# Kernel tuning notes

Hardware: AMD Instinct MI355X
Metric: run time of the kernel (lower is better)

The kernel has to match this reference:

```python
import jax, jax.numpy as jnp
import numpy as np

DIM = 64; N_LAYER = 2; B = 2048; M = 64
N_ENT = 100000; N_REL = 200
TEMP = 0.2; KGE_W = 1e-6
MIN_N = 1e-15; BND = 1e-5


def _norm(x):
    return jnp.sqrt(jnp.clip((x * x).sum(-1, keepdims=True), MIN_N))


def _l2(x):
    # F.normalize(p=2): x / max(||x||, 1e-12)
    return x / jnp.maximum(jnp.sqrt((x * x).sum(-1, keepdims=True)), 1e-12)


def _artanh(x):
    return jnp.arctanh(jnp.clip(x, -1.0 + BND, 1.0 - BND))


def expmap0(u):
    n = _norm(u)
    return jnp.tanh(n) * u / n


def logmap0(x):
    n = _norm(x)
    return _artanh(n) * x / n


def mobius_add(x, y):
    x2 = (x * x).sum(-1, keepdims=True)
    y2 = (y * y).sum(-1, keepdims=True)
    xy = (x * y).sum(-1, keepdims=True)
    num = (1 + 2 * xy + y2) * x + (1 - x2) * y
    den = 1 + 2 * xy + x2 * y2
    return num / jnp.clip(den, MIN_N)


def expmap(u, p):
    lam = 2.0 / jnp.clip(1.0 - (p * p).sum(-1, keepdims=True), MIN_N)
    n = _norm(u)
    return mobius_add(p, jnp.tanh(lam * n / 2.0) * u / n)


def logmap(x, p):
    m = mobius_add(-p, x)
    n = _norm(m)
    lam = 2.0 / jnp.clip(1.0 - (p * p).sum(-1, keepdims=True), MIN_N)
    return (2.0 / lam) * _artanh(n) * m / n


def _ed_agg(h, path, t, att_w1, att_w2):
    # attention: Linear(2d,d,no bias) -> LeakyReLU(0)==ReLU -> Linear(d,1,no bias) -> Sigmoid
    x = jnp.concatenate([h, path], -1)                       # [B,M,2d]
    a = jax.nn.sigmoid(jax.nn.relu(x @ att_w1) @ att_w2)[..., 0]  # [B,M]
    w = jax.nn.softmax(a, axis=-1)
    return (w[..., None] * t).sum(1)                          # [B,d]


def _hyper_agg(h, path, t, curvature, a2_w1, a2_b1, a2_w2, a2_b2):
    h, path, t = _l2(h), _l2(path), _l2(t)
    hh = expmap0(h) * jnp.abs(curvature)
    ht = expmap(t, hh)
    hr = expmap(path, hh)
    tang = logmap0(jnp.concatenate([hh, hr], -1))            # [B,M,2d]
    a = jnp.tanh(jax.nn.relu(tang @ a2_w1 + a2_b1) @ a2_w2 + a2_b2)[..., 0]
    w = jax.nn.softmax(a, axis=-1)                            # [B,M]
    agg = w[..., None] * ht
    mean_pt = (w[..., None] * hh).sum(1, keepdims=True)       # [B,1,d]
    e = logmap(agg, mean_pt)
    return (w[..., None] * e).sum(1)                          # [B,d]


def _build(E, R, h_idx, r_idx, t_idx, init_emb, agg):
    embs = [init_emb]
    for i in range(N_LAYER):
        h = E[h_idx[0]]
        path = R[r_idx[0]]
        for k in range(1, i + 1):  # faithful to source: inner loop reuses index i
            h = h + E[h_idx[i]]
            path = path * R[r_idx[i]]
        embs.append(agg(h, path, E[t_idx[i]]))
    return jnp.stack(embs)  # [L+1, B, d]


def _mlcl(a_stack, b_stack):
    # vectorized over layer index i of MLCL_Loss(a[i], b[i], a_list, b_list)
    na, nb = _l2(a_stack), _l2(b_stack)                       # [L+1,B,d]
    d = na.shape[-1]
    pos = (na * nb).sum(-1)                                   # [L+1,B]
    ttl1 = jnp.einsum('lbd,md->lbm', na, nb.reshape(-1, d))
    ttl2 = jnp.einsum('lbd,md->lbm', nb, na.reshape(-1, d))
    ep = jnp.exp(pos / TEMP)
    l1 = -jnp.log(ep / jnp.exp(ttl1 / TEMP).sum(-1)).sum()
    l2 = -jnp.log(ep / jnp.exp(ttl2 / TEMP).sum(-1)).sum()
    return KGE_W * (l1 + l2)


def _cat_rev(stack):
    # e = stack[0]; for i in 1..L: e = cat(stack[i], e) -> [L, L-1, ..., 0]
    return jnp.concatenate([stack[i] for i in range(stack.shape[0] - 1, -1, -1)], -1)


def setup_inputs() -> dict:
    key = jax.random.key(0)
    ks = jax.random.split(key, 24)
    def ent_idx(k):
        return jax.random.randint(k, (N_LAYER, B, M), 0, N_ENT, dtype=jnp.int32)
    def rel_idx(k):
        return jax.random.randint(k, (N_LAYER, B, M), 0, N_REL, dtype=jnp.int32)
    inp = {
        'items': jax.random.randint(ks[0], (B,), 0, N_ENT, dtype=jnp.int32),
        'ucf_h': ent_idx(ks[1]), 'ucf_r': rel_idx(ks[2]), 'ucf_t': ent_idx(ks[3]),
        'ikg_h': ent_idx(ks[4]), 'ikg_r': rel_idx(ks[5]), 'ikg_t': ent_idx(ks[6]),
        'ukg_h': ent_idx(ks[7]), 'ukg_r': rel_idx(ks[8]), 'ukg_t': ent_idx(ks[9]),
        'icf_h': ent_idx(ks[10]), 'icf_r': rel_idx(ks[11]), 'icf_t': ent_idx(ks[12]),
        'ent_emb': jax.random.normal(ks[13], (N_ENT, DIM), jnp.float32) * 0.02,
        'rel_emb': jax.random.normal(ks[14], (N_REL, DIM), jnp.float32) * 0.02,
        'att_w1': jax.random.normal(ks[15], (2 * DIM, DIM), jnp.float32) * 0.05,
        'att_w2': jax.random.normal(ks[16], (DIM, 1), jnp.float32) * 0.05,
        'att2_w1': jax.random.normal(ks[17], (2 * DIM, DIM), jnp.float32) * 0.05,
        'att2_b1': jnp.zeros((DIM,), jnp.float32),
        'att2_w2': jax.random.normal(ks[18], (DIM, 1), jnp.float32) * 0.05,
        'att2_b2': jnp.zeros((1,), jnp.float32),
        'curvature': jnp.asarray(1.0, jnp.float32),
    }
    return inp


def reference(items, ucf_h, ucf_r, ucf_t, ikg_h, ikg_r, ikg_t,
              ukg_h, ukg_r, ukg_t, icf_h, icf_r, icf_t,
              ent_emb, rel_emb, att_w1, att_w2,
              att2_w1, att2_b1, att2_w2, att2_b2, curvature):
    ed = lambda h, p, t: _ed_agg(h, p, t, att_w1, att_w2)
    hy = lambda h, p, t: _hyper_agg(h, p, t, curvature, att2_w1, att2_b1, att2_w2, att2_b2)
    ucf = _build(ent_emb, rel_emb, ucf_h, ucf_r, ucf_t, ent_emb[ucf_h[0]].mean(1), ed)
    ikg = _build(ent_emb, rel_emb, ikg_h, ikg_r, ikg_t, ent_emb[items], ed)
    ukg = _build(ent_emb, rel_emb, ukg_h, ukg_r, ukg_t, ent_emb[ukg_h[0]].mean(1), hy)
    icf = _build(ent_emb, rel_emb, icf_h, icf_r, icf_t, ent_emb[icf_h[0]].mean(1), hy)
    kge_loss = _mlcl(ucf, ukg) + _mlcl(ikg, icf)
    e_u = jnp.concatenate([_cat_rev(ucf), _cat_rev(ukg)], -1)
    e_i = jnp.concatenate([_cat_rev(icf), _cat_rev(ikg)], -1)
    scores = jax.nn.sigmoid((e_i * e_u).sum(-1))
    return scores, kge_loss
```

## Files before the change

kernel.cpp:

```cpp
#include <hip/hip_runtime.h>
#include <hip/hip_bf16.h>
#include <cstdint>
#include <cstddef>

constexpr int NB = 2048;
constexpr int NM = 64;
constexpr int ND = 64;
constexpr int NBM = NB * NM;
constexpr int NROWS = 3 * NB;
constexpr int STACK = 3 * NB * ND;
constexpr int NZ = 8;

typedef __attribute__((ext_vector_type(8))) short short8;
typedef __attribute__((ext_vector_type(4))) float float4v;

__device__ __forceinline__ float wsum(float v) {
#pragma unroll
  for (int o = 32; o > 0; o >>= 1) v += __shfl_xor(v, o, 64);
  return v;
}

__device__ __forceinline__ float wmax(float v) {
#pragma unroll
  for (int o = 32; o > 0; o >>= 1) v = fmaxf(v, __shfl_xor(v, o, 64));
  return v;
}

__device__ __forceinline__ float rcpf(float x) { return __builtin_amdgcn_rcpf(x); }
__device__ __forceinline__ float sqf(float x) { return __builtin_amdgcn_sqrtf(x); }

__device__ __forceinline__ float fast_tanh(float x) {
  float t = __expf(2.f * x);
  return (t - 1.f) * rcpf(t + 1.f);
}

__device__ __forceinline__ float artanh_clip(float x) {
  x = fminf(fmaxf(x, -1.f + 1e-5f), 1.f - 1e-5f);
  return 0.5f * __logf((1.f + x) * rcpf(1.f - x));
}

__device__ __forceinline__ ushort f2bf(float f) {
  uint u = __float_as_uint(f);
  return (ushort)((u + 0x7FFFu + ((u >> 16) & 1u)) >> 16);
}
__device__ __forceinline__ float bf2f(ushort u) {
  return __uint_as_float((uint)u << 16);
}

__device__ __forceinline__ float readlane_f(float v, int l) {
  return __int_as_float(__builtin_amdgcn_readlane(__float_as_int(v), l));
}

__global__ __launch_bounds__(256) void pack_w1_kernel(
    const float* __restrict__ w1, ushort* __restrict__ out) {
  int e = blockIdx.x * 256 + threadIdx.x;
  if (e >= 8192) return;
  int j = e & 7, ln = (e >> 3) & 63, nt = (e >> 9) & 3, kt = e >> 11;
  int n = nt * 16 + (ln & 15), k = kt * 32 + ((ln >> 4) << 3) + j;
  out[e] = f2bf(w1[k * 64 + n]);
}

__global__ __launch_bounds__(64) void init_item_kernel(
    const float* __restrict__ E, const int* __restrict__ idx, float* __restrict__ out) {
  int b = blockIdx.x, lane = threadIdx.x;
  out[(size_t)b * ND + lane] = E[(size_t)idx[b] * ND + lane];
}

__global__ __launch_bounds__(256) void ed_agg2_kernel(
    const float* __restrict__ E, const float* __restrict__ R,
    const int* __restrict__ h_idx, const int* __restrict__ r_idx,
    const int* __restrict__ t_idx,
    const ushort* __restrict__ w1p, const float* __restrict__ w2,
    float* __restrict__ stack_base, int do_init) {
  __shared__ __align__(16) __hip_bfloat16 xt[64][136];
  __shared__ float a_s[64];
  __shared__ float w_s[64];
  __shared__ float part[4][64];

  const int b = blockIdx.x;
  const int tid = threadIdx.x;
  const int wave = tid >> 6, lane = tid & 63;
  const int m0 = __builtin_amdgcn_readfirstlane(wave) * 16;
  const int colq = lane & 15, quad = lane >> 4;
  const size_t L = (size_t)NB * ND;

  float hd[16], pd[16];

  for (int layer = 0; layer < 2; ++layer) {
    if (layer == 0) {
      float macc = 0.f;
#pragma unroll
      for (int mi = 0; mi < 16; ++mi) {
        const int m = m0 + mi;
        hd[mi] = E[(size_t)h_idx[b * NM + m] * ND + lane];
        pd[mi] = R[(size_t)r_idx[b * NM + m] * ND + lane];
        macc += hd[mi];
        xt[m][lane] = __float2bfloat16(hd[mi]);
        xt[m][64 + lane] = __float2bfloat16(pd[mi]);
      }
      part[wave][lane] = macc;
      __syncthreads();
      if (do_init && wave == 0)
        stack_base[(size_t)b * ND + lane] =
            (part[0][lane] + part[1][lane] + part[2][lane] + part[3][lane]) * (1.f / 64.f);
    } else {
#pragma unroll
      for (int mi = 0; mi < 16; ++mi) {
        const int m = m0 + mi;
        hd[mi] += E[(size_t)h_idx[NBM + b * NM + m] * ND + lane];
        pd[mi] *= R[(size_t)r_idx[NBM + b * NM + m] * ND + lane];
        xt[m][lane] = __float2bfloat16(hd[mi]);
        xt[m][64 + lane] = __float2bfloat16(pd[mi]);
      }
      __syncthreads();
    }

    {
      short8 afr[4];
#pragma unroll
      for (int kt = 0; kt < 4; ++kt)
        afr[kt] = *(const short8*)&xt[m0 + colq][kt * 32 + quad * 8];
      float w2v[4];
#pragma unroll
      for (int nt = 0; nt < 4; ++nt) w2v[nt] = w2[nt * 16 + colq];
      float cc[4][4];
#pragma unroll
      for (int nt = 0; nt < 4; ++nt) {
        float4v c = {0.f, 0.f, 0.f, 0.f};
#pragma unroll
        for (int kt = 0; kt < 4; ++kt) {
          short8 bfr = *(const short8*)&w1p[(((kt << 2) | nt) * 64 + lane) * 8];
          c = __builtin_amdgcn_mfma_f32_16x16x32_bf16(afr[kt], bfr, c, 0, 0, 0);
        }
#pragma unroll
        for (int i = 0; i < 4; ++i) cc[nt][i] = c[i];
      }
      float sred[4];
#pragma unroll
      for (int i = 0; i < 4; ++i)
        sred[i] = fmaxf(cc[0][i], 0.f) * w2v[0] + fmaxf(cc[1][i], 0.f) * w2v[1] +
                  fmaxf(cc[2][i], 0.f) * w2v[2] + fmaxf(cc[3][i], 0.f) * w2v[3];
#pragma unroll
      for (int o = 8; o > 0; o >>= 1) {
#pragma unroll
        for (int i = 0; i < 4; ++i) sred[i] += __shfl_xor(sred[i], o, 64);
      }
      if (colq == 0) {
#pragma unroll
        for (int i = 0; i < 4; ++i)
          a_s[m0 + quad * 4 + i] = 1.f / (1.f + __expf(-sred[i]));
      }
    }
    __syncthreads();
    if (wave == 0) {
      float v = a_s[lane];
      float mx = wmax(v);
      float e = __expf(v - mx);
      float ssum = wsum(e);
      w_s[lane] = e / ssum;
    }
    __syncthreads();

    float o = 0.f;
#pragma unroll
    for (int mi = 0; mi < 16; ++mi) {
      const int m = m0 + mi;
      o = fmaf(w_s[m], E[(size_t)t_idx[(size_t)layer * NBM + b * NM + m] * ND + lane], o);
    }
    part[wave][lane] = o;
    __syncthreads();
    if (wave == 0)
      stack_base[(layer + 1) * L + (size_t)b * ND + lane] =
          part[0][lane] + part[1][lane] + part[2][lane] + part[3][lane];
  }
}

constexpr int OFF_T2 = 0;
constexpr int OFF_P2 = 64 * 72;
constexpr int OFF_H2 = 2 * 64 * 72;
constexpr int XS = 152;
constexpr int OFF_HTS = 64 * XS;
constexpr int REGA_SZ = OFF_HTS + 64 * 72;

__global__ __launch_bounds__(256) void hyper_agg2_kernel(
    const float* __restrict__ E, const float* __restrict__ R,
    const int* __restrict__ h_idx, const int* __restrict__ r_idx,
    const int* __restrict__ t_idx,
    const ushort* __restrict__ w1p, const float* __restrict__ b1,
    const float* __restrict__ w2, const float* __restrict__ b2,
    const float* __restrict__ curv, float* __restrict__ stack_base) {
  __shared__ __align__(16) ushort regA[REGA_SZ];
  __shared__ float dots_s[5][64];
  __shared__ float a_s[64];
  __shared__ float w_s[64];
  __shared__ float meanpt_s[64];
  __shared__ float part[4][64];
  __shared__ float scal;

  const int b = blockIdx.x;
  const int tid = threadIdx.x;
  const int wave = tid >> 6, lane = tid & 63;
  const int m0 = __builtin_amdgcn_readfirstlane(wave) * 16;
  const int colq = lane & 15, quad = lane >> 4;
  const float cabs = fabsf(*curv);
  const size_t L = (size_t)NB * ND;

  float hv[16], pv[16];

  for (int layer = 0; layer < 2; ++layer) {
    if (layer == 0) {
      float macc = 0.f;
#pragma unroll
      for (int mi = 0; mi < 16; ++mi) {
        const int m = m0 + mi;
        hv[mi] = E[(size_t)h_idx[b * NM + m] * ND + lane];
        pv[mi] = R[(size_t)r_idx[b * NM + m] * ND + lane];
        float td = E[(size_t)t_idx[b * NM + m] * ND + lane];
        macc += hv[mi];
        regA[OFF_H2 + m * 72 + lane] = f2bf(hv[mi]);
        regA[OFF_P2 + m * 72 + lane] = f2bf(pv[mi]);
        regA[OFF_T2 + m * 72 + lane] = f2bf(td);
      }
      part[wave][lane] = macc;
      __syncthreads();
      if (wave == 0)
        stack_base[(size_t)b * ND + lane] =
            (part[0][lane] + part[1][lane] + part[2][lane] + part[3][lane]) * (1.f / 64.f);
    } else {
#pragma unroll
      for (int mi = 0; mi < 16; ++mi) {
        const int m = m0 + mi;
        hv[mi] += E[(size_t)h_idx[NBM + b * NM + m] * ND + lane];
        pv[mi] *= R[(size_t)r_idx[NBM + b * NM + m] * ND + lane];
        float td = E[(size_t)t_idx[(size_t)NBM + b * NM + m] * ND + lane];
        regA[OFF_H2 + m * 72 + lane] = f2bf(hv[mi]);
        regA[OFF_P2 + m * 72 + lane] = f2bf(pv[mi]);
        regA[OFF_T2 + m * 72 + lane] = f2bf(td);
      }
      __syncthreads();
    }

    {
      const int fr = m0 + colq;
      const ushort* pH = &regA[OFF_H2 + fr * 72 + quad * 8];
      const ushort* pP = &regA[OFF_P2 + fr * 72 + quad * 8];
      const ushort* pT = &regA[OFF_T2 + fr * 72 + quad * 8];
      short8 h0 = *(const short8*)pH, h1 = *(const short8*)(pH + 32);
      short8 p0 = *(const short8*)pP, p1 = *(const short8*)(pP + 32);
      short8 t0 = *(const short8*)pT, t1 = *(const short8*)(pT + 32);
      const bool dsel = (quad == (colq >> 2));
      const int dr = colq & 3;
#define DIAG_DOT(q, A0, A1, B0, B1)                                         \
      {                                                                      \
        float4v c = {0.f, 0.f, 0.f, 0.f};                                    \
        c = __builtin_amdgcn_mfma_f32_16x16x32_bf16(A0, B0, c, 0, 0, 0);     \
        c = __builtin_amdgcn_mfma_f32_16x16x32_bf16(A1, B1, c, 0, 0, 0);     \
        float dv = (dr & 2) ? ((dr & 1) ? c[3] : c[2])                       \
                            : ((dr & 1) ? c[1] : c[0]);                      \
        if (dsel) dots_s[q][m0 + colq] = dv;                                 \
      }
      DIAG_DOT(0, h0, h1, h0, h1)
      DIAG_DOT(1, p0, p1, p0, p1)
      DIAG_DOT(2, t0, t1, t0, t1)
      DIAG_DOT(3, h0, h1, t0, t1)
      DIAG_DOT(4, h0, h1, p0, p1)
#undef DIAG_DOT
    }
    __syncthreads();

    float g_ch, g_e1, g_e2, g_gh, g_q1, g_q2, g_hts2;
    {
      const int mm = lane;
      float sh = dots_s[0][mm], sp = dots_s[1][mm], st = dots_s[2][mm];
      float sht = dots_s[3][mm], shp = dots_s[4][mm];
      float rih = rcpf(fmaxf(sqf(sh), 1e-12f));
      float rip = rcpf(fmaxf(sqf(sp), 1e-12f));
      float rit = rcpf(fmaxf(sqf(st), 1e-12f));
      float nh = sqf(fmaxf(sh * rih * rih, 1e-15f));
      float ch = fast_tanh(nh) * rcpf(nh) * rih * cabs;
      float p2 = ch * ch * sh;
      float lam = 2.f * rcpf(fmaxf(1.f - p2, 1e-15f));
      float ntn = sqf(fmaxf(st * rit * rit, 1e-15f));
      float ct = fast_tanh(0.5f * lam * ntn) * rcpf(ntn) * rit;
      float y2 = ct * ct * st, xy = ch * ct * sht;
      float At = 1.f + 2.f * xy + y2, Bt = 1.f - p2;
      float rdt = rcpf(fmaxf(1.f + 2.f * xy + p2 * y2, 1e-15f));
      g_e1 = At * ch * rdt;
      g_e2 = Bt * ct * rdt;
      g_hts2 = g_e1 * g_e1 * sh + 2.f * g_e1 * g_e2 * sht + g_e2 * g_e2 * st;
      float npn = sqf(fmaxf(sp * rip * rip, 1e-15f));
      float cp = fast_tanh(0.5f * lam * npn) * rcpf(npn) * rip;
      float z2 = cp * cp * sp, xz = ch * cp * shp;
      float Ar = 1.f + 2.f * xz + z2;
      float rdr = rcpf(fmaxf(1.f + 2.f * xz + p2 * z2, 1e-15f));
      float f1 = Ar * ch * rdr, f2 = Bt * cp * rdr;
      float hr2 = f1 * f1 * sh + 2.f * f1 * f2 * shp + f2 * f2 * sp;
      float n128 = sqf(fmaxf(p2 + hr2, 1e-15f));
      float fq = artanh_clip(n128) * rcpf(n128);
      g_ch = ch;
      g_gh = fq * ch;
      g_q1 = fq * f1;
      g_q2 = fq * f2;
    }

    ushort tr[16];
#pragma unroll
    for (int mi = 0; mi < 16; ++mi)
      tr[mi] = regA[OFF_T2 + (m0 + mi) * 72 + lane];
    __syncthreads();

#pragma unroll
    for (int mi = 0; mi < 16; ++mi) {
      const int m = m0 + mi;
      float tvf = bf2f(tr[mi]);
      float ghm = readlane_f(g_gh, m);
      float q1m = readlane_f(g_q1, m);
      float q2m = readlane_f(g_q2, m);
      float e1m = readlane_f(g_e1, m);
      float e2m = readlane_f(g_e2, m);
      regA[m * XS + lane] = f2bf(ghm * hv[mi]);
      regA[m * XS + 64 + lane] = f2bf(q1m * hv[mi] + q2m * pv[mi]);
      regA[OFF_HTS + m * 72 + lane] = f2bf(e1m * hv[mi] + e2m * tvf);
    }
    __syncthreads();

    {
      short8 afr[4];
#pragma unroll
      for (int kt = 0; kt < 4; ++kt)
        afr[kt] = *(const short8*)&regA[(m0 + colq) * XS + kt * 32 + quad * 8];
      float b1v[4], w2v[4];
#pragma unroll
      for (int nt = 0; nt < 4; ++nt) {
        b1v[nt] = b1[nt * 16 + colq];
        w2v[nt] = w2[nt * 16 + colq];
      }
      float cc[4][4];
#pragma unroll
      for (int nt = 0; nt < 4; ++nt) {
        float4v c = {0.f, 0.f, 0.f, 0.f};
#pragma unroll
        for (int kt = 0; kt < 4; ++kt) {
          short8 bfr = *(const short8*)&w1p[(((kt << 2) | nt) * 64 + lane) * 8];
          c = __builtin_amdgcn_mfma_f32_16x16x32_bf16(afr[kt], bfr, c, 0, 0, 0);
        }
#pragma unroll
        for (int i = 0; i < 4; ++i) cc[nt][i] = c[i];
      }
      float b2v = b2[0];
      float sred[4];
#pragma unroll
      for (int i = 0; i < 4; ++i)
        sred[i] = fmaxf(cc[0][i] + b1v[0], 0.f) * w2v[0] +
                  fmaxf(cc[1][i] + b1v[1], 0.f) * w2v[1] +
                  fmaxf(cc[2][i] + b1v[2], 0.f) * w2v[2] +
                  fmaxf(cc[3][i] + b1v[3], 0.f) * w2v[3];
#pragma unroll
      for (int o = 8; o > 0; o >>= 1) {
#pragma unroll
        for (int i = 0; i < 4; ++i) sred[i] += __shfl_xor(sred[i], o, 64);
      }
      if (colq == 0) {
#pragma unroll
        for (int i = 0; i < 4; ++i)
          a_s[m0 + quad * 4 + i] = fast_tanh(sred[i] + b2v);
      }
    }
    __syncthreads();
    if (wave == 0) {
      float v = a_s[lane];
      float mx = wmax(v);
      float e = __expf(v - mx);
      float ssum = wsum(e);
      w_s[lane] = e / ssum;
    }
    __syncthreads();

    float mp = 0.f;
#pragma unroll
    for (int mi = 0; mi < 16; ++mi) {
      const int m = m0 + mi;
      mp = fmaf(w_s[m] * readlane_f(g_ch, m), hv[mi], mp);
    }
    part[wave][lane] = mp;
    __syncthreads();
    if (wave == 0) {
      float v = part[0][lane] + part[1][lane] + part[2][lane] + part[3][lane];
      meanpt_s[lane] = v;
      float p2m = wsum(v * v);
      if (lane == 0) scal = p2m;
    }
    __syncthreads();

    {
      const ushort* pA = &regA[OFF_HTS + (m0 + colq) * 72 + quad * 8];
      short8 a0 = *(const short8*)pA, a1 = *(const short8*)(pA + 32);
      short8 bm0, bm1;
#pragma unroll
      for (int j = 0; j < 8; ++j) {
        bm0[j] = (short)f2bf(meanpt_s[quad * 8 + j]);
        bm1[j] = (short)f2bf(meanpt_s[32 + quad * 8 + j]);
      }
      float4v c = {0.f, 0.f, 0.f, 0.f};
      c = __builtin_amdgcn_mfma_f32_16x16x32_bf16(a0, bm0, c, 0, 0, 0);
      c = __builtin_amdgcn_mfma_f32_16x16x32_bf16(a1, bm1, c, 0, 0, 0);
      if (colq == 0) {
#pragma unroll
        for (int i = 0; i < 4; ++i) a_s[m0 + quad * 4 + i] = c[i];
      }
    }
    __syncthreads();

    const float p2m = scal;
    const float be = fmaxf(1.f - p2m, 1e-15f);
    float g1, g2;
    {
      const int mm = lane;
      float dpm = a_s[mm];
      float wm = w_s[mm];
      float y2 = wm * wm * g_hts2;
      float xy = -wm * dpm;
      float al = 1.f + 2.f * xy + y2;
      float rd = rcpf(fmaxf(1.f + 2.f * xy + p2m * y2, 1e-15f));
      float md2 = (al * al * p2m - 2.f * al * be * wm * dpm + be * be * y2) * rd * rd;
      float n = sqf(fmaxf(md2, 1e-15f));
      float sm = be * artanh_clip(n) * rcpf(n) * rd;
      g1 = wm * wm * sm * be;
      g2 = wm * sm * al;
    }
    float ovec = 0.f, cA = 0.f;
#pragma unroll
    for (int mi = 0; mi < 16; ++mi) {
      const int m = m0 + mi;
      float htf = bf2f(regA[OFF_HTS + m * 72 + lane]);
      ovec = fmaf(readlane_f(g1, m), htf, ovec);
      cA += readlane_f(g2, m);
    }
    part[wave][lane] = ovec - cA * meanpt_s[lane];
    __syncthreads();
    if (wave == 0)
      stack_base[(layer + 1) * L + (size_t)b * ND + lane] =
          part[0][lane] + part[1][lane] + part[2][lane] + part[3][lane];
  }
}

__global__ __launch_bounds__(256) void l2pos_kernel(
    const float* __restrict__ stacks, __hip_bfloat16* __restrict__ nbf,
    float* __restrict__ pos) {
  int row = blockIdx.x * 4 + (threadIdx.x >> 6);
  int lane = threadIdx.x & 63;
  int sa = blockIdx.y, sb = sa + 2;
  size_t offa = (size_t)sa * STACK + (size_t)row * ND + lane;
  size_t offb = (size_t)sb * STACK + (size_t)row * ND + lane;
  float a = stacks[offa];
  float c = stacks[offb];
  float q0 = a * a, q1 = c * c, q2 = a * c;
#pragma unroll
  for (int o = 32; o > 0; o >>= 1) {
    q0 += __shfl_xor(q0, o, 64);
    q1 += __shfl_xor(q1, o, 64);
    q2 += __shfl_xor(q2, o, 64);
  }
  float ra = rcpf(fmaxf(sqf(q0), 1e-12f));
  float rc = rcpf(fmaxf(sqf(q1), 1e-12f));
  nbf[offa] = __float2bfloat16(a * ra);
  nbf[offb] = __float2bfloat16(c * rc);
  if (lane == 0) pos[sa * NROWS + row] = q2 * ra * rc;
}

__global__ __launch_bounds__(256) void lse_mfma_kernel(
    const ushort* __restrict__ nbf, float* __restrict__ Spart) {
  __shared__ __align__(16) ushort ytile[2][64 * 72];
  const int tid = threadIdx.x;
  const int wave = tid >> 6, lane = tid & 63;
  const int pair = blockIdx.y;
  const int z = blockIdx.z;
  int xi = (pair & 2) ? ((pair & 1) ? 3 : 1) : ((pair & 1) ? 2 : 0);
  int yi = xi ^ 2;
  const ushort* X = nbf + (size_t)xi * STACK;
  const ushort* Y = nbf + (size_t)yi * STACK;
  const int r0 = blockIdx.x * 64 + wave * 16;
  const int row = lane & 15, quad = lane >> 4;

  short8 a0 = *(const short8*)&X[(size_t)(r0 + row) * 64 + quad * 8];
  short8 a1 = *(const short8*)&X[(size_t)(r0 + row) * 64 + 32 + quad * 8];

  const int srow = tid >> 2, schunk = tid & 3;
  constexpr int NT = (NROWS / NZ) / 64;
  const int c0 = z * (NROWS / NZ);
  const ushort* sg = &Y[(size_t)(c0 + srow) * 64 + schunk * 16];
  ushort* sl = &ytile[0][0] + srow * 72 + schunk * 16;

  {
    short8 s0 = *(const short8*)sg;
    short8 s1 = *(const short8*)(sg + 8);
// ... 21 lines not shown
      c = __builtin_amdgcn_mfma_f32_16x16x32_bf16(a1, b1, c, 0, 0, 0);
#pragma unroll
      for (int i = 0; i < 4; ++i) rsum[i] += __expf(c[i] * 5.f);
    }
    if (ct + 1 < NT) {
      ushort* dst = &ytile[0][0] + ((ct + 1) & 1) * (64 * 72) + srow * 72 + schunk * 16;
      *(short8*)dst = n0;
      *(short8*)(dst + 8) = n1;
      __syncthreads();
    }
  }
#pragma unroll
  for (int i = 0; i < 4; ++i) {
    float v = rsum[i];
    v += __shfl_xor(v, 1, 64);
    v += __shfl_xor(v, 2, 64);
    v += __shfl_xor(v, 4, 64);
    v += __shfl_xor(v, 8, 64);
    if (row == 0)
      Spart[((size_t)z * 4 + pair) * NROWS + r0 + quad * 4 + i] = v;
  }
}

__global__ __launch_bounds__(256) void scores_kernel(
    const float* __restrict__ stacks, float* __restrict__ out) {
  int b = blockIdx.x * 4 + (threadIdx.x >> 6);
  int lane = threadIdx.x & 63;
  float s = 0.f;
#pragma unroll
  for (int l = 0; l < 3; ++l) {
    size_t o = (size_t)l * NB * ND + (size_t)b * ND + lane;
    s += stacks[0 * (size_t)STACK + o] * stacks[3 * (size_t)STACK + o]
       + stacks[2 * (size_t)STACK + o] * stacks[1 * (size_t)STACK + o];
  }
  s = wsum(s);
  if (lane == 0) out[b] = 1.f / (1.f + __expf(-s));
}

__global__ __launch_bounds__(256) void loss_part_kernel(
    const float* __restrict__ Spart, const float* __restrict__ pos,
    double* __restrict__ lossp) {
  __shared__ double red[256];
  const int t = threadIdx.x, blk = blockIdx.x;
  double acc = 0.0;
#pragma unroll
  for (int r = 0; r < 2; ++r) {
    int i = blk * 512 + r * 256 + t;
    float s = 0.f;
#pragma unroll
    for (int zz = 0; zz < NZ; ++zz) s += Spart[i + zz * 4 * NROWS];
    acc += (double)__logf(s);
  }
  {
    int j = blk * 256 + t;
    acc -= 10.0 * (double)pos[j];
  }
  red[t] = acc;
  __syncthreads();
  for (int s = 128; s > 0; s >>= 1) {
    if (t < s) red[t] += red[t + s];
    __syncthreads();
  }
  if (t == 0) lossp[blk] = red[0];
}

__global__ __launch_bounds__(64) void loss_final_kernel(
    const double* __restrict__ lossp, float* __restrict__ out) {
  int lane = threadIdx.x;
  double v = (lane < 48) ? lossp[lane] : 0.0;
#pragma unroll
  for (int o = 32; o > 0; o >>= 1) v += __shfl_xor(v, o, 64);
  if (lane == 0) out[NB] = (float)(1e-6 * v);
}

extern "C" void kernel_launch(void* const* d_in, const int* in_sizes, int n_in,
                              void* d_out, int out_size, void* d_ws, size_t ws_size,
                              hipStream_t stream) {
  const int* items = (const int*)d_in[0];
  const int* ucf_h = (const int*)d_in[1];
  const int* ucf_r = (const int*)d_in[2];
  const int* ucf_t = (const int*)d_in[3];
  const int* ikg_h = (const int*)d_in[4];
  const int* ikg_r = (const int*)d_in[5];
  const int* ikg_t = (const int*)d_in[6];
  const int* ukg_h = (const int*)d_in[7];
  const int* ukg_r = (const int*)d_in[8];
  const int* ukg_t = (const int*)d_in[9];
  const int* icf_h = (const int*)d_in[10];
  const int* icf_r = (const int*)d_in[11];
  const int* icf_t = (const int*)d_in[12];
  const float* E = (const float*)d_in[13];
  const float* R = (const float*)d_in[14];
  const float* att_w1 = (const float*)d_in[15];
  const float* att_w2 = (const float*)d_in[16];
  const float* a2_w1 = (const float*)d_in[17];
  const float* a2_b1 = (const float*)d_in[18];
  const float* a2_w2 = (const float*)d_in[19];
  const float* a2_b2 = (const float*)d_in[20];
  const float* curv = (const float*)d_in[21];
  float* outp = (float*)d_out;

  float* ws = (float*)d_ws;
  float* stacks = ws;
  float* Spart = stacks + 4 * (size_t)STACK;
  float* posarr = Spart + (size_t)NZ * 4 * NROWS;
  __hip_bfloat16* nbf = (__hip_bfloat16*)(posarr + 2 * (size_t)NROWS);
  ushort* w1p_ed = (ushort*)(nbf + 4 * (size_t)STACK);
  ushort* w1p_hy = w1p_ed + 8192;
  double* lossp = (double*)(w1p_hy + 8192);

  float* ucf = stacks + 0 * (size_t)STACK;
  float* ikg = stacks + 1 * (size_t)STACK;
  float* ukg = stacks + 2 * (size_t)STACK;
  float* icf = stacks + 3 * (size_t)STACK;

  pack_w1_kernel<<<32, 256, 0, stream>>>(att_w1, w1p_ed);
  pack_w1_kernel<<<32, 256, 0, stream>>>(a2_w1, w1p_hy);

  init_item_kernel<<<NB, 64, 0, stream>>>(E, items, ikg);

  ed_agg2_kernel<<<NB, 256, 0, stream>>>(E, R, ucf_h, ucf_r, ucf_t, w1p_ed, att_w2, ucf, 1);
  ed_agg2_kernel<<<NB, 256, 0, stream>>>(E, R, ikg_h, ikg_r, ikg_t, w1p_ed, att_w2, ikg, 0);
  hyper_agg2_kernel<<<NB, 256, 0, stream>>>(E, R, ukg_h, ukg_r, ukg_t, w1p_hy, a2_b1, a2_w2, a2_b2, curv, ukg);
  hyper_agg2_kernel<<<NB, 256, 0, stream>>>(E, R, icf_h, icf_r, icf_t, w1p_hy, a2_b1, a2_w2, a2_b2, curv, icf);

  l2pos_kernel<<<dim3(NROWS / 4, 2), 256, 0, stream>>>(stacks, nbf, posarr);
  lse_mfma_kernel<<<dim3(NROWS / 64, 4, NZ), 256, 0, stream>>>((const ushort*)nbf, Spart);

  scores_kernel<<<NB / 4, 256, 0, stream>>>(stacks, outp);
  loss_part_kernel<<<48, 256, 0, stream>>>(Spart, posarr, lossp);
  loss_final_kernel<<<1, 64, 0, stream>>>(lossp, outp);
}
```

Measured before the change: 363.2 us.

## Fuse four aggregation kernels into one launch with packed bf16 register state

Replaces the two ed_agg and two hyper_agg launches with a single kernel on a 2D grid whose y dimension selects the family. The h/p state is held as packed bf16 pairs in registers rather than fp32 arrays, shared-memory layout is compacted, and the diagonal dot products move from a shared-memory round trip to shuffles. Launch bounds request 5 blocks per SM. The aim is to cut launch gaps, let the four families overlap, and raise occupancy. In exchange, layer-2 inputs are rounded to bf16 before accumulation, and the branch between families adds divergence within the single kernel.

```diff
diff --git a/kernel.cpp b/kernel.cpp
--- a/kernel.cpp
+++ b/kernel.cpp
@@ -66,381 +66,370 @@
   out[(size_t)b * ND + lane] = E[(size_t)idx[b] * ND + lane];
 }
 
-__global__ __launch_bounds__(256) void ed_agg2_kernel(
+constexpr int OFF_H = 0;
+constexpr int OFF_P = 4608;
+constexpr int OFF_T = 9728;
+constexpr int XS = 152;
+constexpr int REGA_SZ = 14336;
+
+__global__ __launch_bounds__(256, 5) void agg_all_kernel(
     const float* __restrict__ E, const float* __restrict__ R,
-    const int* __restrict__ h_idx, const int* __restrict__ r_idx,
-    const int* __restrict__ t_idx,
-    const ushort* __restrict__ w1p, const float* __restrict__ w2,
-    float* __restrict__ stack_base, int do_init) {
-  __shared__ __align__(16) __hip_bfloat16 xt[64][136];
+    const int* __restrict__ h0, const int* __restrict__ r0, const int* __restrict__ t0,
+    const int* __restrict__ h1, const int* __restrict__ r1, const int* __restrict__ t1,
+    const int* __restrict__ h2, const int* __restrict__ r2, const int* __restrict__ t2,
+    const int* __restrict__ h3, const int* __restrict__ r3, const int* __restrict__ t3,
+    const ushort* __restrict__ w1p_ed, const float* __restrict__ w2_ed,
+    const ushort* __restrict__ w1p_hy, const float* __restrict__ b1,
+    const float* __restrict__ w2_hy, const float* __restrict__ b2,
+    const float* __restrict__ curv,
+    float* __restrict__ s_ucf, float* __restrict__ s_ikg,
+    float* __restrict__ s_ukg, float* __restrict__ s_icf) {
+  __shared__ __align__(16) ushort regA[REGA_SZ];
   __shared__ float a_s[64];
   __shared__ float w_s[64];
+  __shared__ float meanpt_s[64];
   __shared__ float part[4][64];
+  __shared__ float scal;
 
   const int b = blockIdx.x;
+  const int fam = blockIdx.y;
   const int tid = threadIdx.x;
   const int wave = tid >> 6, lane = tid & 63;
   const int m0 = __builtin_amdgcn_readfirstlane(wave) * 16;
   const int colq = lane & 15, quad = lane >> 4;
   const size_t L = (size_t)NB * ND;
 
-  float hd[16], pd[16];
-
-  for (int layer = 0; layer < 2; ++layer) {
-    if (layer == 0) {
-      float macc = 0.f;
+  const int* h_idx = (fam == 0) ? h0 : (fam == 1) ? h1 : (fam == 2) ? h2 : h3;
+  const int* r_idx = (fam == 0) ? r0 : (fam == 1) ? r1 : (fam == 2) ? r2 : r3;
+  const int* t_idx = (fam == 0) ? t0 : (fam == 1) ? t1 : (fam == 2) ? t2 : t3;
+  float* sb = (fam == 0) ? s_ucf : (fam == 1) ? s_ikg : (fam == 2) ? s_ukg : s_icf;
+
+  uint hp[16];
+
+  if (fam < 2) {
+    const int do_init = (fam == 0);
+    for (int layer = 0; layer < 2; ++layer) {
+      if (layer == 0) {
+        float macc = 0.f;
+#pragma unroll
+        for (int mi = 0; mi < 16; ++mi) {
+          const int m = m0 + mi;
+          float hd = E[(size_t)h_idx[b * NM + m] * ND + lane];
+          float pd = R[(size_t)r_idx[b * NM + m] * ND + lane];
+          macc += hd;
+          ushort hb = f2bf(hd), pb = f2bf(pd);
+          hp[mi] = (uint)hb | ((uint)pb << 16);
+          regA[m * XS + lane] = hb;
+          regA[m * XS + 64 + lane] = pb;
+        }
+        part[wave][lane] = macc;
+      } else {
+#pragma unroll
+        for (int mi = 0; mi < 16; ++mi) {
+          const int m = m0 + mi;
+          float hd = bf2f((ushort)hp[mi]) + E[(size_t)h_idx[NBM + b * NM + m] * ND + lane];
+          float pd = bf2f((ushort)(hp[mi] >> 16)) * R[(size_t)r_idx[NBM + b * NM + m] * ND + lane];
+          ushort hb = f2bf(hd), pb = f2bf(pd);
+          hp[mi] = (uint)hb | ((uint)pb << 16);
+          regA[m * XS + lane] = hb;
+          regA[m * XS + 64 + lane] = pb;
+        }
+      }
+
+      {
+        short8 afr[4];
+#pragma unroll
+        for (int kt = 0; kt < 4; ++kt)
+          afr[kt] = *(const short8*)&regA[(m0 + colq) * XS + kt * 32 + quad * 8];
+        float w2v[4];
+#pragma unroll
+        for (int nt = 0; nt < 4; ++nt) w2v[nt] = w2_ed[nt * 16 + colq];
+        float cc[4][4];
+#pragma unroll
+        for (int nt = 0; nt < 4; ++nt) {
+          float4v c = {0.f, 0.f, 0.f, 0.f};
+#pragma unroll
+          for (int kt = 0; kt < 4; ++kt) {
+            short8 bfr = *(const short8*)&w1p_ed[(((kt << 2) | nt) * 64 + lane) * 8];
+            c = __builtin_amdgcn_mfma_f32_16x16x32_bf16(afr[kt], bfr, c, 0, 0, 0);
+          }
+#pragma unroll
+          for (int i = 0; i < 4; ++i) cc[nt][i] = c[i];
+        }
+        float sred[4];
+#pragma unroll
+        for (int i = 0; i < 4; ++i)
+          sred[i] = fmaxf(cc[0][i], 0.f) * w2v[0] + fmaxf(cc[1][i], 0.f) * w2v[1] +
+                    fmaxf(cc[2][i], 0.f) * w2v[2] + fmaxf(cc[3][i], 0.f) * w2v[3];
+#pragma unroll
+        for (int o = 8; o > 0; o >>= 1) {
+#pragma unroll
+          for (int i = 0; i < 4; ++i) sred[i] += __shfl_xor(sred[i], o, 64);
+        }
+        if (colq == 0) {
+#pragma unroll
+          for (int i = 0; i < 4; ++i)
+            a_s[m0 + quad * 4 + i] = 1.f / (1.f + __expf(-sred[i]));
+        }
+      }
+      __syncthreads();
+      if (wave == 0) {
+        if (layer == 0 && do_init)
+          sb[(size_t)b * ND + lane] =
+              (part[0][lane] + part[1][lane] + part[2][lane] + part[3][lane]) * (1.f / 64.f);
+        float v = a_s[lane];
+        float mx = wmax(v);
+        float e = __expf(v - mx);
+        float ssum = wsum(e);
+        w_s[lane] = e / ssum;
+      }
+      __syncthreads();
+
+      float o = 0.f;
 #pragma unroll
       for (int mi = 0; mi < 16; ++mi) {
         const int m = m0 + mi;
-        hd[mi] = E[(size_t)h_idx[b * NM + m] * ND + lane];
-        pd[mi] = R[(size_t)r_idx[b * NM + m] * ND + lane];
-        macc += hd[mi];
-        xt[m][lane] = __float2bfloat16(hd[mi]);
-        xt[m][64 + lane] = __float2bfloat16(pd[mi]);
-      }
-      part[wave][lane] = macc;
-      __syncthreads();
-      if (do_init && wave == 0)
-        stack_base[(size_t)b * ND + lane] =
+        o = fmaf(w_s[m], E[(size_t)t_idx[(size_t)layer * NBM + b * NM + m] * ND + lane], o);
+      }
+      part[wave][lane] = o;
+      __syncthreads();
+      if (wave == 0)
+        sb[(layer + 1) * L + (size_t)b * ND + lane] =
+            part[0][lane] + part[1][lane] + part[2][lane] + part[3][lane];
+      if (layer == 0) __syncthreads();
+    }
+  } else {
+    const float cabs = fabsf(*curv);
+    const int j = colq;
+    const int srcl = ((j >> 2) << 4) + j;
+
+    for (int layer = 0; layer < 2; ++layer) {
+      if (layer == 0) {
+        float macc = 0.f;
+#pragma unroll
+        for (int mi = 0; mi < 16; ++mi) {
+          const int m = m0 + mi;
+          float hd = E[(size_t)h_idx[b * NM + m] * ND + lane];
+          float pd = R[(size_t)r_idx[b * NM + m] * ND + lane];
+          float td = E[(size_t)t_idx[b * NM + m] * ND + lane];
+          macc += hd;
+          ushort hb = f2bf(hd), pb = f2bf(pd);
+          hp[mi] = (uint)hb | ((uint)pb << 16);
+          regA[OFF_H + m * 72 + lane] = hb;
+          regA[OFF_P + m * 72 + lane] = pb;
+          regA[OFF_T + m * 72 + lane] = f2bf(td);
+        }
+        part[wave][lane] = macc;
+      } else {
+#pragma unroll
+        for (int mi = 0; mi < 16; ++mi) {
+          const int m = m0 + mi;
+          float hd = bf2f((ushort)hp[mi]) + E[(size_t)h_idx[NBM + b * NM + m] * ND + lane];
+          float pd = bf2f((ushort)(hp[mi] >> 16)) * R[(size_t)r_idx[NBM + b * NM + m] * ND + lane];
+          float td = E[(size_t)t_idx[(size_t)NBM + b * NM + m] * ND + lane];
+          ushort hb = f2bf(hd), pb = f2bf(pd);
+          hp[mi] = (uint)hb | ((uint)pb << 16);
+          regA[OFF_H + m * 72 + lane] = hb;
+          regA[OFF_P + m * 72 + lane] = pb;
+          regA[OFF_T + m * 72 + lane] = f2bf(td);
+        }
+      }
+
+      float sh, sp, st, sht, shp;
+      {
+        const int fr = m0 + colq;
+        const ushort* pH = &regA[OFF_H + fr * 72 + quad * 8];
+        const ushort* pP = &regA[OFF_P + fr * 72 + quad * 8];
+        const ushort* pT = &regA[OFF_T + fr * 72 + quad * 8];
+        short8 hh0 = *(const short8*)pH, hh1 = *(const short8*)(pH + 32);
+        short8 pp0 = *(const short8*)pP, pp1 = *(const short8*)(pP + 32);
+        short8 tt0 = *(const short8*)pT, tt1 = *(const short8*)(pT + 32);
+        const int dr = colq & 3;
+#define DIAG_DOT(OUTV, A0, A1, B0, B1)                                      \
+        {                                                                    \
+          float4v c = {0.f, 0.f, 0.f, 0.f};                                  \
+          c = __builtin_amdgcn_mfma_f32_16x16x32_bf16(A0, B0, c, 0, 0, 0);   \
+          c = __builtin_amdgcn_mfma_f32_16x16x32_bf16(A1, B1, c, 0, 0, 0);   \
+          float dv = (dr & 2) ? ((dr & 1) ? c[3] : c[2])                     \
+                              : ((dr & 1) ? c[1] : c[0]);                    \
+          OUTV = __shfl(dv, srcl, 64);                                       \
+        }
+        DIAG_DOT(sh, hh0, hh1, hh0, hh1)
+        DIAG_DOT(sp, pp0, pp1, pp0, pp1)
+        DIAG_DOT(st, tt0, tt1, tt0, tt1)
+        DIAG_DOT(sht, hh0, hh1, tt0, tt1)
+        DIAG_DOT(shp, hh0, hh1, pp0, pp1)
+#undef DIAG_DOT
+      }
+
+      float g_ch, g_e1, g_e2, g_gh, g_q1, g_q2, g_hts2;
+      {
+        float rih = rcpf(fmaxf(sqf(sh), 1e-12f));
+        float rip = rcpf(fmaxf(sqf(sp), 1e-12f));
+        float rit = rcpf(fmaxf(sqf(st), 1e-12f));
+        float nh = sqf(fmaxf(sh * rih * rih, 1e-15f));
+        float ch = fast_tanh(nh) * rcpf(nh) * rih * cabs;
+        float p2 = ch * ch * sh;
+        float lam = 2.f * rcpf(fmaxf(1.f - p2, 1e-15f));
+        float ntn = sqf(fmaxf(st * rit * rit, 1e-15f));
+        float ct = fast_tanh(0.5f * lam * ntn) * rcpf(ntn) * rit;
+        float y2 = ct * ct * st, xy = ch * ct * sht;
+        float At = 1.f + 2.f * xy + y2, Bt = 1.f - p2;
+        float rdt = rcpf(fmaxf(1.f + 2.f * xy + p2 * y2, 1e-15f));
+        g_e1 = At * ch * rdt;
+        g_e2 = Bt * ct * rdt;
+        g_hts2 = g_e1 * g_e1 * sh + 2.f * g_e1 * g_e2 * sht + g_e2 * g_e2 * st;
+        float npn = sqf(fmaxf(sp * rip * rip, 1e-15f));
+        float cp = fast_tanh(0.5f * lam * npn) * rcpf(npn) * rip;
+        float z2 = cp * cp * sp, xz = ch * cp * shp;
+        float Ar = 1.f + 2.f * xz + z2;
+        float rdr = rcpf(fmaxf(1.f + 2.f * xz + p2 * z2, 1e-15f));
+        float f1 = Ar * ch * rdr, f2 = Bt * cp * rdr;
+        float hr2 = f1 * f1 * sh + 2.f * f1 * f2 * shp + f2 * f2 * sp;
+        float n128 = sqf(fmaxf(p2 + hr2, 1e-15f));
+        float fq = artanh_clip(n128) * rcpf(n128);
+        g_ch = ch;
+        g_gh = fq * ch;
+        g_q1 = fq * f1;
+        g_q2 = fq * f2;
+      }
+
+      __syncthreads();
+      if (layer == 0 && wave == 0)
+        sb[(size_t)b * ND + lane] =
             (part[0][lane] + part[1][lane] + part[2][lane] + part[3][lane]) * (1.f / 64.f);
-    } else {
+
 #pragma unroll
       for (int mi = 0; mi < 16; ++mi) {
         const int m = m0 + mi;
-        hd[mi] += E[(size_t)h_idx[NBM + b * NM + m] * ND + lane];
-        pd[mi] *= R[(size_t)r_idx[NBM + b * NM + m] * ND + lane];
-        xt[m][lane] = __float2bfloat16(hd[mi]);
-        xt[m][64 + lane] = __float2bfloat16(pd[mi]);
-      }
-      __syncthreads();
-    }
-
-    {
-      short8 afr[4];
-#pragma unroll
-      for (int kt = 0; kt < 4; ++kt)
-        afr[kt] = *(const short8*)&xt[m0 + colq][kt * 32 + quad * 8];
-      float w2v[4];
-#pragma unroll
-      for (int nt = 0; nt < 4; ++nt) w2v[nt] = w2[nt * 16 + colq];
-      float cc[4][4];
-#pragma unroll
-      for (int nt = 0; nt < 4; ++nt) {
-        float4v c = {0.f, 0.f, 0.f, 0.f};
-#pragma unroll
-        for (int kt = 0; kt < 4; ++kt) {
-          short8 bfr = *(const short8*)&w1p[(((kt << 2) | nt) * 64 + lane) * 8];
-          c = __builtin_amdgcn_mfma_f32_16x16x32_bf16(afr[kt], bfr, c, 0, 0, 0);
-        }
-#pragma unroll
-        for (int i = 0; i < 4; ++i) cc[nt][i] = c[i];
-      }
-      float sred[4];
-#pragma unroll
-      for (int i = 0; i < 4; ++i)
-        sred[i] = fmaxf(cc[0][i], 0.f) * w2v[0] + fmaxf(cc[1][i], 0.f) * w2v[1] +
-                  fmaxf(cc[2][i], 0.f) * w2v[2] + fmaxf(cc[3][i], 0.f) * w2v[3];
-#pragma unroll
-      for (int o = 8; o > 0; o >>= 1) {
-#pragma unroll
-        for (int i = 0; i < 4; ++i) sred[i] += __shfl_xor(sred[i], o, 64);
-      }
-      if (colq == 0) {
+        float hvf = bf2f((ushort)hp[mi]);
+        float pvf = bf2f((ushort)(hp[mi] >> 16));
+        float tvf = bf2f(regA[OFF_T + m * 72 + lane]);
+        float ghm = readlane_f(g_gh, mi);
+        float q1m = readlane_f(g_q1, mi);
+        float q2m = readlane_f(g_q2, mi);
+        float e1m = readlane_f(g_e1, mi);
+        float e2m = readlane_f(g_e2, mi);
+        regA[m * XS + lane] = f2bf(ghm * hvf);
+        regA[m * XS + 64 + lane] = f2bf(q1m * hvf + q2m * pvf);
+        regA[OFF_T + m * 72 + lane] = f2bf(e1m * hvf + e2m * tvf);
+      }
+
+      {
+        short8 afr[4];
+#pragma unroll
+        for (int kt = 0; kt < 4; ++kt)
+          afr[kt] = *(const short8*)&regA[(m0 + colq) * XS + kt * 32 + quad * 8];
+        float b1v[4], w2v[4];
+#pragma unroll
+        for (int nt = 0; nt < 4; ++nt) {
+          b1v[nt] = b1[nt * 16 + colq];
+          w2v[nt] = w2_hy[nt * 16 + colq];
+        }
+        float cc[4][4];
+#pragma unroll
+        for (int nt = 0; nt < 4; ++nt) {
+          float4v c = {0.f, 0.f, 0.f, 0.f};
+#pragma unroll
+          for (int kt = 0; kt < 4; ++kt) {
+            short8 bfr = *(const short8*)&w1p_hy[(((kt << 2) | nt) * 64 + lane) * 8];
+            c = __builtin_amdgcn_mfma_f32_16x16x32_bf16(afr[kt], bfr, c, 0, 0, 0);
+          }
+#pragma unroll
+          for (int i = 0; i < 4; ++i) cc[nt][i] = c[i];
+        }
+        float b2v = b2[0];
+        float sred[4];
 #pragma unroll
         for (int i = 0; i < 4; ++i)
-          a_s[m0 + quad * 4 + i] = 1.f / (1.f + __expf(-sred[i]));
-      }
-    }
-    __syncthreads();
-    if (wave == 0) {
-      float v = a_s[lane];
-      float mx = wmax(v);
-      float e = __expf(v - mx);
-      float ssum = wsum(e);
-      w_s[lane] = e / ssum;
-    }
-    __syncthreads();
-
-    float o = 0.f;
-#pragma unroll
-    for (int mi = 0; mi < 16; ++mi) {
-      const int m = m0 + mi;
-      o = fmaf(w_s[m], E[(size_t)t_idx[(size_t)layer * NBM + b * NM + m] * ND + lane], o);
-    }
-    part[wave][lane] = o;
-    __syncthreads();
-    if (wave == 0)
-      stack_base[(layer + 1) * L + (size_t)b * ND + lane] =
-          part[0][lane] + part[1][lane] + part[2][lane] + part[3][lane];
-  }
-}
-
-constexpr int OFF_T2 = 0;
-constexpr int OFF_P2 = 64 * 72;
-constexpr int OFF_H2 = 2 * 64 * 72;
-constexpr int XS = 152;
-constexpr int OFF_HTS = 64 * XS;
-constexpr int REGA_SZ = OFF_HTS + 64 * 72;
-
-__global__ __launch_bounds__(256) void hyper_agg2_kernel(
-    const float* __restrict__ E, const float* __restrict__ R,
-    const int* __restrict__ h_idx, const int* __restrict__ r_idx,
-    const int* __restrict__ t_idx,
-    const ushort* __restrict__ w1p, const float* __restrict__ b1,
-    const float* __restrict__ w2, const float* __restrict__ b2,
-    const float* __restrict__ curv, float* __restrict__ stack_base) {
-  __shared__ __align__(16) ushort regA[REGA_SZ];
-  __shared__ float dots_s[5][64];
-  __shared__ float a_s[64];
-  __shared__ float w_s[64];
-  __shared__ float meanpt_s[64];
-  __shared__ float part[4][64];
-  __shared__ float scal;
-
-  const int b = blockIdx.x;
-  const int tid = threadIdx.x;
-  const int wave = tid >> 6, lane = tid & 63;
-  const int m0 = __builtin_amdgcn_readfirstlane(wave) * 16;
-  const int colq = lane & 15, quad = lane >> 4;
-  const float cabs = fabsf(*curv);
-  const size_t L = (size_t)NB * ND;
-
-  float hv[16], pv[16];
-
-  for (int layer = 0; layer < 2; ++layer) {
-    if (layer == 0) {
-      float macc = 0.f;
+          sred[i] = fmaxf(cc[0][i] + b1v[0], 0.f) * w2v[0] +
+                    fmaxf(cc[1][i] + b1v[1], 0.f) * w2v[1] +
+                    fmaxf(cc[2][i] + b1v[2], 0.f) * w2v[2] +
+                    fmaxf(cc[3][i] + b1v[3], 0.f) * w2v[3];
+#pragma unroll
+        for (int o = 8; o > 0; o >>= 1) {
+#pragma unroll
+          for (int i = 0; i < 4; ++i) sred[i] += __shfl_xor(sred[i], o, 64);
+        }
+        if (colq == 0) {
+#pragma unroll
+          for (int i = 0; i < 4; ++i)
+            a_s[m0 + quad * 4 + i] = fast_tanh(sred[i] + b2v);
+        }
+      }
+      __syncthreads();
+      if (wave == 0) {
+        float v = a_s[lane];
+        float mx = wmax(v);
+        float e = __expf(v - mx);
+        float ssum = wsum(e);
+        w_s[lane] = e / ssum;
+      }
+      __syncthreads();
+
+      float mp = 0.f;
 #pragma unroll
       for (int mi = 0; mi < 16; ++mi) {
         const int m = m0 + mi;
-        hv[mi] = E[(size_t)h_idx[b * NM + m] * ND + lane];
-        pv[mi] = R[(size_t)r_idx[b * NM + m] * ND + lane];
-        float td = E[(size_t)t_idx[b * NM + m] * ND + lane];
-        macc += hv[mi];
-        regA[OFF_H2 + m * 72 + lane] = f2bf(hv[mi]);
-        regA[OFF_P2 + m * 72 + lane] = f2bf(pv[mi]);
-        regA[OFF_T2 + m * 72 + lane] = f2bf(td);
-      }
-      part[wave][lane] = macc;
-      __syncthreads();
-      if (wave == 0)
-        stack_base[(size_t)b * ND + lane] =
-            (part[0][lane] + part[1][lane] + part[2][lane] + part[3][lane]) * (1.f / 64.f);
-    } else {
+        mp = fmaf(w_s[m] * readlane_f(g_ch, mi), bf2f((ushort)hp[mi]), mp);
+      }
+      part[wave][lane] = mp;
+      __syncthreads();
+      if (wave == 0) {
+        float v = part[0][lane] + part[1][lane] + part[2][lane] + part[3][lane];
+        meanpt_s[lane] = v;
+        float p2m = wsum(v * v);
+        if (lane == 0) scal = p2m;
+      }
+      __syncthreads();
+
+      float dpv;
+      {
+        const ushort* pA = &regA[OFF_T + (m0 + colq) * 72 + quad * 8];
+        short8 a0 = *(const short8*)pA, a1 = *(const short8*)(pA + 32);
+        short8 bm0, bm1;
+#pragma unroll
+        for (int jj = 0; jj < 8; ++jj) {
+          bm0[jj] = (short)f2bf(meanpt_s[quad * 8 + jj]);
+          bm1[jj] = (short)f2bf(meanpt_s[32 + quad * 8 + jj]);
+        }
+        float4v c = {0.f, 0.f, 0.f, 0.f};
+        c = __builtin_amdgcn_mfma_f32_16x16x32_bf16(a0, bm0, c, 0, 0, 0);
+        c = __builtin_amdgcn_mfma_f32_16x16x32_bf16(a1, bm1, c, 0, 0, 0);
+        const int dr = colq & 3;
+        float dv = (dr & 2) ? ((dr & 1) ? c[3] : c[2]) : ((dr & 1) ? c[1] : c[0]);
+        dpv = __shfl(dv, srcl, 64);
+      }
+
+      const float p2m = scal;
+      const float be = fmaxf(1.f - p2m, 1e-15f);
+      float g1, g2;
+      {
+        float wm = w_s[m0 + j];
+        float y2 = wm * wm * g_hts2;
+        float xy = -wm * dpv;
+        float al = 1.f + 2.f * xy + y2;
+        float rd = rcpf(fmaxf(1.f + 2.f * xy + p2m * y2, 1e-15f));
+        float md2 = (al * al * p2m - 2.f * al * be * wm * dpv + be * be * y2) * rd * rd;
+        float n = sqf(fmaxf(md2, 1e-15f));
+        float sm = be * artanh_clip(n) * rcpf(n) * rd;
+        g1 = wm * wm * sm * be;
+        g2 = wm * sm * al;
+      }
+      float ovec = 0.f, cA = 0.f;
 #pragma unroll
       for (int mi = 0; mi < 16; ++mi) {
         const int m = m0 + mi;
-        hv[mi] += E[(size_t)h_idx[NBM + b * NM + m] * ND + lane];
-        pv[mi] *= R[(size_t)r_idx[NBM + b * NM + m] * ND + lane];
-        float td = E[(size_t)t_idx[(size_t)NBM + b * NM + m] * ND + lane];
-        regA[OFF_H2 + m * 72 + lane] = f2bf(hv[mi]);
-        regA[OFF_P2 + m * 72 + lane] = f2bf(pv[mi]);
-        regA[OFF_T2 + m * 72 + lane] = f2bf(td);
-      }
-      __syncthreads();
+        float htf = bf2f(regA[OFF_T + m * 72 + lane]);
+        ovec = fmaf(readlane_f(g1, mi), htf, ovec);
+        cA += readlane_f(g2, mi);
+      }
+      part[wave][lane] = ovec - cA * meanpt_s[lane];
+      __syncthreads();
+      if (wave == 0)
+        sb[(layer + 1) * L + (size_t)b * ND + lane] =
+            part[0][lane] + part[1][lane] + part[2][lane] + part[3][lane];
     }
-
-    {
-      const int fr = m0 + colq;
-      const ushort* pH = &regA[OFF_H2 + fr * 72 + quad * 8];
-      const ushort* pP = &regA[OFF_P2 + fr * 72 + quad * 8];
-      const ushort* pT = &regA[OFF_T2 + fr * 72 + quad * 8];
-      short8 h0 = *(const short8*)pH, h1 = *(const short8*)(pH + 32);
-      short8 p0 = *(const short8*)pP, p1 = *(const short8*)(pP + 32);
-      short8 t0 = *(const short8*)pT, t1 = *(const short8*)(pT + 32);
-      const bool dsel = (quad == (colq >> 2));
-      const int dr = colq & 3;
-#define DIAG_DOT(q, A0, A1, B0, B1)                                         \
-      {                                                                      \
-        float4v c = {0.f, 0.f, 0.f, 0.f};                                    \
-        c = __builtin_amdgcn_mfma_f32_16x16x32_bf16(A0, B0, c, 0, 0, 0);     \
-        c = __builtin_amdgcn_mfma_f32_16x16x32_bf16(A1, B1, c, 0, 0, 0);     \
-        float dv = (dr & 2) ? ((dr & 1) ? c[3] : c[2])                       \
-                            : ((dr & 1) ? c[1] : c[0]);                      \
-        if (dsel) dots_s[q][m0 + colq] = dv;                                 \
-      }
-      DIAG_DOT(0, h0, h1, h0, h1)
-      DIAG_DOT(1, p0, p1, p0, p1)
-      DIAG_DOT(2, t0, t1, t0, t1)
-      DIAG_DOT(3, h0, h1, t0, t1)
-      DIAG_DOT(4, h0, h1, p0, p1)
-#undef DIAG_DOT
-    }
-    __syncthreads();
-
-    float g_ch, g_e1, g_e2, g_gh, g_q1, g_q2, g_hts2;
-    {
-      const int mm = lane;
-      float sh = dots_s[0][mm], sp = dots_s[1][mm], st = dots_s[2][mm];
-      float sht = dots_s[3][mm], shp = dots_s[4][mm];
-      float rih = rcpf(fmaxf(sqf(sh), 1e-12f));
-      float rip = rcpf(fmaxf(sqf(sp), 1e-12f));
-      float rit = rcpf(fmaxf(sqf(st), 1e-12f));
-      float nh = sqf(fmaxf(sh * rih * rih, 1e-15f));
-      float ch = fast_tanh(nh) * rcpf(nh) * rih * cabs;
-      float p2 = ch * ch * sh;
-      float lam = 2.f * rcpf(fmaxf(1.f - p2, 1e-15f));
-      float ntn = sqf(fmaxf(st * rit * rit, 1e-15f));
-      float ct = fast_tanh(0.5f * lam * ntn) * rcpf(ntn) * rit;
-      float y2 = ct * ct * st, xy = ch * ct * sht;
-      float At = 1.f + 2.f * xy + y2, Bt = 1.f - p2;
-      float rdt = rcpf(fmaxf(1.f + 2.f * xy + p2 * y2, 1e-15f));
-      g_e1 = At * ch * rdt;
-      g_e2 = Bt * ct * rdt;
-      g_hts2 = g_e1 * g_e1 * sh + 2.f * g_e1 * g_e2 * sht + g_e2 * g_e2 * st;
-      float npn = sqf(fmaxf(sp * rip * rip, 1e-15f));
-      float cp = fast_tanh(0.5f * lam * npn) * rcpf(npn) * rip;
-      float z2 = cp * cp * sp, xz = ch * cp * shp;
-      float Ar = 1.f + 2.f * xz + z2;
-      float rdr = rcpf(fmaxf(1.f + 2.f * xz + p2 * z2, 1e-15f));
-      float f1 = Ar * ch * rdr, f2 = Bt * cp * rdr;
-      float hr2 = f1 * f1 * sh + 2.f * f1 * f2 * shp + f2 * f2 * sp;
-      float n128 = sqf(fmaxf(p2 + hr2, 1e-15f));
-      float fq = artanh_clip(n128) * rcpf(n128);
-      g_ch = ch;
-      g_gh = fq * ch;
-      g_q1 = fq * f1;
-      g_q2 = fq * f2;
-    }
-
-    ushort tr[16];
-#pragma unroll
-    for (int mi = 0; mi < 16; ++mi)
-      tr[mi] = regA[OFF_T2 + (m0 + mi) * 72 + lane];
-    __syncthreads();
-
-#pragma unroll
-    for (int mi = 0; mi < 16; ++mi) {
-      const int m = m0 + mi;
-      float tvf = bf2f(tr[mi]);
-      float ghm = readlane_f(g_gh, m);
-      float q1m = readlane_f(g_q1, m);
-      float q2m = readlane_f(g_q2, m);
-      float e1m = readlane_f(g_e1, m);
-      float e2m = readlane_f(g_e2, m);
-      regA[m * XS + lane] = f2bf(ghm * hv[mi]);
-      regA[m * XS + 64 + lane] = f2bf(q1m * hv[mi] + q2m * pv[mi]);
-      regA[OFF_HTS + m * 72 + lane] = f2bf(e1m * hv[mi] + e2m * tvf);
-    }
-    __syncthreads();
-
-    {
-      short8 afr[4];
-#pragma unroll
-      for (int kt = 0; kt < 4; ++kt)
-        afr[kt] = *(const short8*)&regA[(m0 + colq) * XS + kt * 32 + quad * 8];
-      float b1v[4], w2v[4];
-#pragma unroll
-      for (int nt = 0; nt < 4; ++nt) {
-        b1v[nt] = b1[nt * 16 + colq];
-        w2v[nt] = w2[nt * 16 + colq];
-      }
-      float cc[4][4];
-#pragma unroll
-      for (int nt = 0; nt < 4; ++nt) {
-        float4v c = {0.f, 0.f, 0.f, 0.f};
-#pragma unroll
-        for (int kt = 0; kt < 4; ++kt) {
-          short8 bfr = *(const short8*)&w1p[(((kt << 2) | nt) * 64 + lane) * 8];
-          c = __builtin_amdgcn_mfma_f32_16x16x32_bf16(afr[kt], bfr, c, 0, 0, 0);
-        }
-#pragma unroll
-        for (int i = 0; i < 4; ++i) cc[nt][i] = c[i];
-      }
-      float b2v = b2[0];
-      float sred[4];
-#pragma unroll
-      for (int i = 0; i < 4; ++i)
-        sred[i] = fmaxf(cc[0][i] + b1v[0], 0.f) * w2v[0] +
-                  fmaxf(cc[1][i] + b1v[1], 0.f) * w2v[1] +
-                  fmaxf(cc[2][i] + b1v[2], 0.f) * w2v[2] +
-                  fmaxf(cc[3][i] + b1v[3], 0.f) * w2v[3];
-#pragma unroll
-      for (int o = 8; o > 0; o >>= 1) {
-#pragma unroll
-        for (int i = 0; i < 4; ++i) sred[i] += __shfl_xor(sred[i], o, 64);
-      }
-      if (colq == 0) {
-#pragma unroll
-        for (int i = 0; i < 4; ++i)
-          a_s[m0 + quad * 4 + i] = fast_tanh(sred[i] + b2v);
-      }
-    }
-    __syncthreads();
-    if (wave == 0) {
-      float v = a_s[lane];
-      float mx = wmax(v);
-      float e = __expf(v - mx);
-      float ssum = wsum(e);
-      w_s[lane] = e / ssum;
-    }
-    __syncthreads();
-
-    float mp = 0.f;
-#pragma unroll
-    for (int mi = 0; mi < 16; ++mi) {
-      const int m = m0 + mi;
-      mp = fmaf(w_s[m] * readlane_f(g_ch, m), hv[mi], mp);
-    }
-    part[wave][lane] = mp;
-    __syncthreads();
-    if (wave == 0) {
-      float v = part[0][lane] + part[1][lane] + part[2][lane] + part[3][lane];
-      meanpt_s[lane] = v;
-      float p2m = wsum(v * v);
-      if (lane == 0) scal = p2m;
-    }
-    __syncthreads();
-
-    {
-      const ushort* pA = &regA[OFF_HTS + (m0 + colq) * 72 + quad * 8];
-      short8 a0 = *(const short8*)pA, a1 = *(const short8*)(pA + 32);
-      short8 bm0, bm1;
-#pragma unroll
-      for (int j = 0; j < 8; ++j) {
-        bm0[j] = (short)f2bf(meanpt_s[quad * 8 + j]);
-        bm1[j] = (short)f2bf(meanpt_s[32 + quad * 8 + j]);
-      }
-      float4v c = {0.f, 0.f, 0.f, 0.f};
-      c = __builtin_amdgcn_mfma_f32_16x16x32_bf16(a0, bm0, c, 0, 0, 0);
-      c = __builtin_amdgcn_mfma_f32_16x16x32_bf16(a1, bm1, c, 0, 0, 0);
-      if (colq == 0) {
-#pragma unroll
-        for (int i = 0; i < 4; ++i) a_s[m0 + quad * 4 + i] = c[i];
-      }
-    }
-    __syncthreads();
-
-    const float p2m = scal;
-    const float be = fmaxf(1.f - p2m, 1e-15f);
-    float g1, g2;
-    {
-      const int mm = lane;
-      float dpm = a_s[mm];
-      float wm = w_s[mm];
-      float y2 = wm * wm * g_hts2;
-      float xy = -wm * dpm;
-      float al = 1.f + 2.f * xy + y2;
-      float rd = rcpf(fmaxf(1.f + 2.f * xy + p2m * y2, 1e-15f));
-      float md2 = (al * al * p2m - 2.f * al * be * wm * dpm + be * be * y2) * rd * rd;
-      float n = sqf(fmaxf(md2, 1e-15f));
-      float sm = be * artanh_clip(n) * rcpf(n) * rd;
-      g1 = wm * wm * sm * be;
-      g2 = wm * sm * al;
-    }
-    float ovec = 0.f, cA = 0.f;
-#pragma unroll
-    for (int mi = 0; mi < 16; ++mi) {
-      const int m = m0 + mi;
-      float htf = bf2f(regA[OFF_HTS + m * 72 + lane]);
-      ovec = fmaf(readlane_f(g1, m), htf, ovec);
-      cA += readlane_f(g2, m);
-    }
-    part[wave][lane] = ovec - cA * meanpt_s[lane];
-    __syncthreads();
-    if (wave == 0)
-      stack_base[(layer + 1) * L + (size_t)b * ND + lane] =
-          part[0][lane] + part[1][lane] + part[2][lane] + part[3][lane];
   }
 }
 
@@ -568,8 +557,8 @@
     acc += (double)__logf(s);
   }
   {
-    int j = blk * 256 + t;
-    acc -= 10.0 * (double)pos[j];
+    int jj = blk * 256 + t;
+    acc -= 10.0 * (double)pos[jj];
   }
   red[t] = acc;
   __syncthreads();
@@ -635,10 +624,12 @@
 
   init_item_kernel<<<NB, 64, 0, stream>>>(E, items, ikg);
 
-  ed_agg2_kernel<<<NB, 256, 0, stream>>>(E, R, ucf_h, ucf_r, ucf_t, w1p_ed, att_w2, ucf, 1);
-  ed_agg2_kernel<<<NB, 256, 0, stream>>>(E, R, ikg_h, ikg_r, ikg_t, w1p_ed, att_w2, ikg, 0);
-  hyper_agg2_kernel<<<NB, 256, 0, stream>>>(E, R, ukg_h, ukg_r, ukg_t, w1p_hy, a2_b1, a2_w2, a2_b2, curv, ukg);
-  hyper_agg2_kernel<<<NB, 256, 0, stream>>>(E, R, icf_h, icf_r, icf_t, w1p_hy, a2_b1, a2_w2, a2_b2, curv, icf);
+  agg_all_kernel<<<dim3(NB, 4), 256, 0, stream>>>(
+      E, R,
+      ucf_h, ucf_r, ucf_t, ikg_h, ikg_r, ikg_t,
+      ukg_h, ukg_r, ukg_t, icf_h, icf_r, icf_t,
+      w1p_ed, att_w2, w1p_hy, a2_b1, a2_w2, a2_b2, curv,
+      ucf, ikg, ukg, icf);
 
   l2pos_kernel<<<dim3(NROWS / 4, 2), 256, 0, stream>>>(stacks, nbf, posarr);
   lse_mfma_kernel<<<dim3(NROWS / 64, 4, NZ), 256, 0, stream>>>((const ushort*)nbf, Spart);
```

New measurement: 586.7 us. 61.5% more time.
